# Kernel tuning notes

Hardware: AMD Instinct MI355X
Metric: run time of the kernel (lower is better)

Reference implementation:

```python
import jax, jax.numpy as jnp
import numpy as np

N = 50000          # nodes
E = 1_600_000      # edges (avg degree 32)
D = 128            # in_channels
H = 128            # hidden_channels
B = 4096           # batch_nodes
BETA = 0.5


def setup_inputs() -> dict:
    key = jax.random.key(0)
    ks = jax.random.split(key, 12)
    s = 1.0 / np.sqrt(D)
    inp = {
        "x": jax.random.normal(ks[0], (N, D), jnp.float32),
        "edge_index": jax.random.randint(ks[1], (2, E), 0, N, dtype=jnp.int64),
        "batch_nodes": jax.random.randint(ks[2], (B,), 0, N, dtype=jnp.int64),
        "labels": jax.random.randint(ks[3], (N,), 0, 2, dtype=jnp.int64),
        # GCNConv layer params (weight [in,out], bias [out])
        "W1": jax.random.uniform(ks[4], (D, H), jnp.float32, -s, s),
        "b1": jnp.zeros((H,), jnp.float32),
        "W2": jax.random.uniform(ks[5], (H, H), jnp.float32, -s, s),
        "b2": jnp.zeros((H,), jnp.float32),
        # Bilinear heads: weight [H,H] (out_features=1), scalar bias
        "W_ctx": jax.random.uniform(ks[6], (H, H), jnp.float32, -s, s),
        "b_ctx": jnp.zeros((), jnp.float32),
        "W_loc": jax.random.uniform(ks[7], (H, H), jnp.float32, -s, s),
        "b_loc": jnp.zeros((), jnp.float32),
    }
    return inp


def _gcn_conv(h, W, b, src, dst, n):
    """PyG GCNConv: linear transform, add self-loops, sym-normalized scatter-add."""
    h = h @ W  # [n, out]
    loop = jnp.arange(n, dtype=src.dtype)
    src_f = jnp.concatenate([src, loop])
    dst_f = jnp.concatenate([dst, loop])
    deg = jax.ops.segment_sum(jnp.ones_like(dst_f, dtype=h.dtype), dst_f, num_segments=n)
    dinv = jnp.where(deg > 0, jax.lax.rsqrt(deg), 0.0)
    norm = dinv[src_f] * dinv[dst_f]                      # [E+n]
    msg = h[src_f] * norm[:, None]                        # gather + scale
    out = jax.ops.segment_sum(msg, dst_f, num_segments=n)  # scatter-add
    return out + b


def _bce_logits(z, y):
    # mean(softplus(z) - z*y) == BCEWithLogits
    return jnp.mean(jax.nn.softplus(z) - z * y)


def reference(x, edge_index, batch_nodes, labels, W1, b1, W2, b2, W_ctx, b_ctx, W_loc, b_loc):
    src, dst = edge_index[0], edge_index[1]
    n = x.shape[0]
    layers = [(W1, b1), (W2, b2)]

    # eval mode: dropout is identity
    h = x
    for W, b in layers:
        h = jax.nn.relu(_gcn_conv(h, W, b, src, dst, n))

    gf = h[batch_nodes]                                   # [B, H]
    y = (labels[batch_nodes] == 1).astype(gf.dtype)       # [B]
    pos_cnt = jnp.sum(y)
    neg_cnt = y.shape[0] - pos_cnt
    pos_proto = (y[:, None] * gf).sum(0) / pos_cnt        # [H]

    # context bilinear head: z_i = gf_i^T W_ctx pos_proto + b (neg_sim is dead code in source)
    pos_sim = gf @ (W_ctx @ pos_proto) + b_ctx            # [B]
    ctx_loss = _bce_logits(pos_sim, y)

    # environment view: zero out batch nodes, re-run GCN stack (no dropout in source)
    masked_x = x.at[batch_nodes].set(0.0)
    env_h = masked_x
    for W, b in layers:
        env_h = jax.nn.relu(_gcn_conv(env_h, W, b, src, dst, n))
    env_f = env_h[batch_nodes]                            # [B, H]

    local_sim = jnp.einsum('nd,de,ne->n', env_f, W_loc, gf) + b_loc
    local_loss = _bce_logits(local_sim, 1.0 - y)

    total_loss = BETA * ctx_loss + (1.0 - BETA) * local_loss
    # source's guard: both classes present (true w.h.p. for random labels)
    total_loss = jnp.where((pos_cnt > 0) & (neg_cnt > 0), total_loss, 0.0)
    return gf, total_loss
```

## Files before the change

kernel.cpp:

```cpp
#include <hip/hip_runtime.h>
#include <math.h>

#define HID 128
#define CAP 12288
#define NBUCK_MAX 256
#define EPB 8192

typedef _Float16 h2v __attribute__((ext_vector_type(2)));
typedef _Float16 h8v __attribute__((ext_vector_type(8)));
typedef float f4v __attribute__((ext_vector_type(4)));

static inline int ceil_div(int a, int b) { return (a + b - 1) / b; }


__global__ __launch_bounds__(256) void k_setup(const float* __restrict__ W1, const float* __restrict__ W2,
                                               const float* __restrict__ Wl, _Float16* T1, _Float16* T2,
                                               _Float16* Tl, unsigned int* mask, int* bcur,
                                               float* part, float* pcnt_raw, float* lsums, int mw, int NB) {
    int b = blockIdx.x;
    int t = threadIdx.x;
    if (b < 192) {
        int which = b >> 6;
        int idx = (b & 63) * 256 + t;
        int k = idx >> 7, c = idx & 127;
        const float* S = (which == 0) ? W1 : ((which == 1) ? W2 : Wl);
        _Float16* D = (which == 0) ? T1 : ((which == 1) ? T2 : Tl);
        D[c * 128 + k] = (_Float16)S[idx];
    } else {
        int i = (b - 192) * 256 + t;
        if (i < mw) mask[i] = 0u;
        if (i < NB) bcur[i] = i * CAP;
        if (b == 192) {
            if (t < 128) part[t] = 0.f;
            else if (t == 128) pcnt_raw[0] = 0.f;
            else if (t < 131) lsums[t - 129] = 0.f;
        }
    }
}


__global__ __launch_bounds__(1024) void k_partA(const int* __restrict__ ei, int* __restrict__ bcur,
                                                unsigned int* __restrict__ ebuf,
                                                const int* __restrict__ batch, unsigned int* mask,
                                                int E, int B, int NB, int NBLKE) {
    if ((int)blockIdx.x >= NBLKE) {
        int i = ((int)blockIdx.x - NBLKE) * 1024 + threadIdx.x;
        if (i < B) { int nd = batch[i]; atomicOr(&mask[nd >> 5], 1u << (nd & 31)); }
        return;
    }
    __shared__ int lcnt[NBUCK_MAX];
    __shared__ int sc[NBUCK_MAX];
    __shared__ int lcur[NBUCK_MAX];
    __shared__ int gbase[NBUCK_MAX];
    __shared__ unsigned int se[EPB];
    int tid = threadIdx.x;
    if (tid < NBUCK_MAX) lcnt[tid] = 0;
    __syncthreads();
    int base = blockIdx.x * EPB;
    unsigned int pk[8];
    int bk[8];
#pragma unroll
    for (int j = 0; j < 8; ++j) {
        int e = base + tid + j * 1024;
        if (e < E) {
            int s = ei[e], d = ei[E + e];
            pk[j] = ((unsigned int)s << 8) | (unsigned int)(d & 255);
            bk[j] = d >> 8;
            atomicAdd(&lcnt[bk[j]], 1);
        } else bk[j] = -1;
    }
    __syncthreads();
    if (tid < NBUCK_MAX) sc[tid] = lcnt[tid];
    __syncthreads();
    for (int off = 1; off < NBUCK_MAX; off <<= 1) {
        int v = 0;
        if (tid < NBUCK_MAX && tid >= off) v = sc[tid - off];
        __syncthreads();
        if (tid < NBUCK_MAX) sc[tid] += v;
        __syncthreads();
    }
    if (tid < NBUCK_MAX) {
        int cc = lcnt[tid];
        int lo = sc[tid] - cc;
        lcur[tid] = lo;
        gbase[tid] = cc ? atomicAdd(&bcur[tid], cc) : 0;
    }
    __syncthreads();
#pragma unroll
    for (int j = 0; j < 8; ++j) {
        if (bk[j] >= 0) {
            int r = atomicAdd(&lcur[bk[j]], 1);
            se[r] = pk[j];
        }
    }
    __syncthreads();
    int wid = tid >> 6, lane = tid & 63;
    for (int b = wid; b < NB; b += 16) {
        int cc = lcnt[b];
        int lo = sc[b] - cc;
        int go = gbase[b];
        for (int i = lane; i < cc; i += 64) ebuf[go + i] = se[lo + i];
    }
}


__global__ __launch_bounds__(256) void k_csr(const unsigned int* __restrict__ ebuf, const int* __restrict__ bcur,
                                             const unsigned int* __restrict__ mask,
                                             float* __restrict__ sdinv, int* __restrict__ rs,
                                             int* __restrict__ degpk, unsigned int* __restrict__ csr, int N) {
    __shared__ unsigned int se[CAP];
    __shared__ int deg[256];
    __shared__ int fde[256];
    __shared__ int sc[256];
    __shared__ int cu[256];
    __shared__ int cf[256];
    int b = blockIdx.x, t = threadIdx.x;
    deg[t] = 0; fde[t] = 0;
    __syncthreads();
    int base = b * CAP;
    int ecnt = bcur[b] - base;
    for (int i = t; i < ecnt; i += 256) {
        unsigned int v = ebuf[base + i];
        int s = v >> 8;
        int fl = (mask[s >> 5] >> (s & 31)) & 1;
        se[i] = ((unsigned int)s << 9) | ((unsigned int)fl << 8) | (v & 255);
        atomicAdd(&deg[v & 255], 1);
        if (fl) atomicAdd(&fde[v & 255], 1);
    }
    __syncthreads();
    int dv = deg[t], fv = fde[t];
    int pv = (dv + 7) & ~7;
    sc[t] = pv;
    __syncthreads();
    for (int off = 1; off < 256; off <<= 1) {
        int v2 = (t >= off) ? sc[t - off] : 0;
        __syncthreads();
        sc[t] += v2;
        __syncthreads();
    }
    int r0 = base + sc[t] - pv;
    cu[t] = r0;
    cf[t] = r0 + (dv - fv);
    int node = b * 256 + t;
    if (node < N) {
        rs[node] = r0;
        degpk[node] = dv | (fv << 16);
        float di = rsqrtf((float)(dv + 1));
        if ((mask[node >> 5] >> (node & 31)) & 1) di = -di;
        sdinv[node] = di;
    }
    __syncthreads();
    for (int i = t; i < ecnt; i += 256) {
        unsigned int v = se[i];
        int d8 = v & 255;
        int p = ((v >> 8) & 1) ? atomicAdd(&cf[d8], 1) : atomicAdd(&cu[d8], 1);
        csr[p] = v >> 9;
    }
    if (node < N) {
        for (int j = dv; j < pv; ++j) csr[r0 + j] = (unsigned int)N;
    }
}


__global__ __launch_bounds__(256) void k_cast(const float* __restrict__ x, const float* __restrict__ sdinv,
                                              _Float16* __restrict__ xs, _Float16* __restrict__ H, int N) {
    int i = blockIdx.x * 256 + threadIdx.x;
    int nx = N * 16;
    if (i < nx) {
        int node = i >> 4;
        float da = fabsf(sdinv[node]);
        int o = i * 8;
        float4 a = *(const float4*)&x[o];
        float4 b = *(const float4*)&x[o + 4];
        h8v v;
        v[0] = (_Float16)(a.x * da); v[1] = (_Float16)(a.y * da);
        v[2] = (_Float16)(a.z * da); v[3] = (_Float16)(a.w * da);
        v[4] = (_Float16)(b.x * da); v[5] = (_Float16)(b.y * da);
        v[6] = (_Float16)(b.z * da); v[7] = (_Float16)(b.w * da);
        *(h8v*)&xs[o] = v;
    } else if (i < nx + 16) {
        *(h8v*)&xs[(size_t)i * 8] = (h8v){};
    } else if (i < nx + 16 + 32) {
        int j = i - (nx + 16);
        *(h8v*)&H[(size_t)2 * N * HID + j * 8] = (h8v){};
    }
}


__global__ __launch_bounds__(512) void k_layer1(const _Float16* __restrict__ xs, const int* __restrict__ rs,
                                                const int* __restrict__ degpk, const unsigned int* __restrict__ csr,
                                                const float* __restrict__ sdinv, const _Float16* __restrict__ W1T,
                                                const float* __restrict__ bias, _Float16* __restrict__ H, int N) {
    __shared__ __align__(16) _Float16 sWT[128 * 136];
    __shared__ __align__(16) _Float16 sAgg[64 * 136];
    __shared__ float sbias[128];
    __shared__ float sda[32];
    float* sC = (float*)sWT;

    int tid = threadIdx.x;
    int wave = tid >> 6, lane = tid & 63;
    int grp = lane >> 4, rl = lane & 15;

#pragma unroll
    for (int it = 0; it < 4; ++it) {
        int lin = (it * 512 + tid) * 8;
        int c = lin >> 7, k = lin & 127;
        *(h8v*)&sWT[c * 136 + k] = *(const h8v*)&W1T[lin];
    }
    if (tid < 128) sbias[tid] = bias[tid];
    if (tid < 32) {
        int nd = blockIdx.x * 32 + tid;
        sda[tid] = (nd < N) ? fabsf(sdinv[nd]) : 0.f;
    }

    int ch = rl * 8;
    int lg = wave * 4 + grp;
    int row = blockIdx.x * 32 + lg;
    bool ok = row < N;
    int p = 0, deg = 0, fd = 0;
    float sd = 0.f;
    h8v hs = {};
    if (ok) {
        p = rs[row];
        int dp = degpk[row];
        deg = dp & 0xffff; fd = dp >> 16;
        sd = sdinv[row];
        hs = *(const h8v*)&xs[(size_t)row * HID + ch];
    }
    int ud = deg - fd;
    int pd = (deg + 7) & ~7;
    int t1 = max(pd, __shfl_xor(pd, 16));
    int m  = max(t1, __shfl_xor(t1, 32));
    float U[8] = {}, F[8] = {};
    for (int i = 0; i < m; i += 16) {
        int id[16];
#pragma unroll
        for (int k = 0; k < 16; ++k) {
            int raw = (int)csr[p + i + k];
            id[k] = (i + k < pd) ? raw : N;
        }
        h8v h[16];
#pragma unroll
        for (int k = 0; k < 16; ++k) h[k] = *(const h8v*)&xs[(size_t)id[k] * HID + ch];
        h8v s0 = (h[0] + h[1]) + (h[2] + h[3]);
        h8v s1 = (h[4] + h[5]) + (h[6] + h[7]);
        h8v s2 = (h[8] + h[9]) + (h[10] + h[11]);
        h8v s3 = (h[12] + h[13]) + (h[14] + h[15]);
        h8v s  = (s0 + s1) + (s2 + s3);
#pragma unroll
        for (int j = 0; j < 8; ++j) U[j] += (float)s[j];
        if (i + 16 > ud) {
#pragma unroll
            for (int k = 0; k < 16; ++k) {
                if (i + k >= ud && i + k < deg) {
#pragma unroll
                    for (int j = 0; j < 8; ++j) F[j] += (float)h[k][j];
                }
            }
        }
    }
    {
        float da = fabsf(sd);
        float keep = (sd < 0.f) ? 0.f : 1.f;
        h8v lo = {}, hi = {};
        if (ok) {
#pragma unroll
            for (int j = 0; j < 8; ++j) {
                float f = (float)hs[j];
                lo[j] = (_Float16)(da * (U[j] + f));
                hi[j] = (_Float16)(da * (U[j] - F[j] + keep * f));
            }
        }
        *(h8v*)&sAgg[(2 * lg) * 136 + ch] = lo;
        *(h8v*)&sAgg[(2 * lg + 1) * 136 + ch] = hi;
    }
    __syncthreads();

    int g = lane >> 4;
    int rowtile = (wave & 3) * 16;
    int colbase = (wave >> 2) * 64;
    f4v acc[4];
#pragma unroll
    for (int cc = 0; cc < 4; ++cc) acc[cc] = (f4v){0.f, 0.f, 0.f, 0.f};
#pragma unroll
    for (int kb = 0; kb < 4; ++kb) {
        int k0 = kb * 32 + g * 8;
        h8v av = *(const h8v*)&sAgg[(rowtile + rl) * 136 + k0];
#pragma unroll
        for (int cc = 0; cc < 4; ++cc) {
            h8v bv = *(const h8v*)&sWT[(colbase + cc * 16 + rl) * 136 + k0];
            acc[cc] = __builtin_amdgcn_mfma_f32_16x16x32_f16(bv, av, acc[cc], 0, 0, 0);
        }
    }
    __syncthreads();

    int lrow = rowtile + rl;
    float dsc = sda[lrow >> 1];
#pragma unroll
    for (int cc = 0; cc < 4; ++cc) {
        f4v v = acc[cc];
        int col = colbase + cc * 16 + g * 4;
#pragma unroll
        for (int i2 = 0; i2 < 4; ++i2) v[i2] = fmaxf(v[i2] + sbias[col + i2], 0.f) * dsc;
        *(f4v*)&sC[lrow * 132 + col] = v;
    }
    __syncthreads();

    int sr = tid >> 3, ck = tid & 7;
    int gRow = blockIdx.x * 64 + sr;
    if (gRow < 2 * N) {
        const float* src = &sC[sr * 132 + ck * 16];
        h8v o0, o1;
#pragma unroll
        for (int j = 0; j < 8; ++j) { o0[j] = (_Float16)src[j]; o1[j] = (_Float16)src[8 + j]; }
        _Float16* dst = &H[(size_t)gRow * HID + ck * 16];
        *(h8v*)&dst[0] = o0;
        *(h8v*)&dst[8] = o1;
    }
}


__global__ __launch_bounds__(256) void k_layer2(const _Float16* __restrict__ H, const int* __restrict__ rs,
                                                const int* __restrict__ degpk, const unsigned int* __restrict__ csr,
                                                const float* __restrict__ sdinv, const int* __restrict__ batch,
                                                const int* __restrict__ labels,
                                                const _Float16* __restrict__ W2T, const float* __restrict__ bias,
                                                float* __restrict__ gf, _Float16* __restrict__ envh,
                                                float* __restrict__ yv, float* __restrict__ part,
                                                float* __restrict__ pcnt_raw, int B, int N) {
    __shared__ __align__(16) _Float16 sWT[128 * 136];
    __shared__ __align__(16) _Float16 sAgg[32 * 136];
    __shared__ float sbias[128];
    __shared__ float sy2[16];
    float* sC = (float*)sWT;

    int tid = threadIdx.x;
    int wave = tid >> 6, lane = tid & 63;
    int grp = lane >> 4, rl = lane & 15;

#pragma unroll
    for (int it = 0; it < 8; ++it) {
        int lin = (it * 256 + tid) * 8;
        int c = lin >> 7, k = lin & 127;
        *(h8v*)&sWT[c * 136 + k] = *(const h8v*)&W2T[lin];
    }
    if (tid < 128) sbias[tid] = bias[tid];

    int ch = rl * 8;
    int lg = wave * 4 + grp;
    int ri = blockIdx.x * 16 + lg;
    bool ok = ri < B;
    int p = 0, deg = 0, row = 0;
    float da = 0.f;
    h8v hn = {}, he = {};
    if (ok) {
        row = batch[ri];
        p = rs[row];
        deg = degpk[row] & 0xffff;
        da = fabsf(sdinv[row]);
        hn = *(const h8v*)&H[(size_t)row * 256 + ch];
        he = *(const h8v*)&H[(size_t)row * 256 + 128 + ch];
    }
    int pd = (deg + 7) & ~7;
    int t1 = max(pd, __shfl_xor(pd, 16));
    int m  = max(t1, __shfl_xor(t1, 32));
    float a[8] = {}, e[8] = {};
    for (int i = 0; i < m; i += 8) {
        int id[8];
#pragma unroll
        for (int k = 0; k < 8; ++k) {
            int raw = (int)csr[p + i + k];
            id[k] = (i + k < pd) ? raw : N;
        }
        h8v xn[8], xe[8];
#pragma unroll
        for (int k = 0; k < 8; ++k) {
            xn[k] = *(const h8v*)&H[(size_t)id[k] * 256 + ch];
            xe[k] = *(const h8v*)&H[(size_t)id[k] * 256 + 128 + ch];
        }
        h8v sn = ((xn[0] + xn[1]) + (xn[2] + xn[3])) + ((xn[4] + xn[5]) + (xn[6] + xn[7]));
        h8v sv = ((xe[0] + xe[1]) + (xe[2] + xe[3])) + ((xe[4] + xe[5]) + (xe[6] + xe[7]));
#pragma unroll
        for (int j = 0; j < 8; ++j) { a[j] += (float)sn[j]; e[j] += (float)sv[j]; }
    }
    {
        h8v lo = {}, hi = {};
        if (ok) {
#pragma unroll
            for (int j = 0; j < 8; ++j) {
                lo[j] = (_Float16)(da * (a[j] + (float)hn[j]));
                hi[j] = (_Float16)(da * (e[j] + (float)he[j]));
            }
        }
        *(h8v*)&sAgg[(2 * lg) * 136 + ch] = lo;
        *(h8v*)&sAgg[(2 * lg + 1) * 136 + ch] = hi;
    }
    __syncthreads();

    int g = lane >> 4;
    int rowtile = (wave & 1) * 16;
    int colbase = (wave >> 1) * 64;
    f4v acc[4];
#pragma unroll
    for (int cc = 0; cc < 4; ++cc) acc[cc] = (f4v){0.f, 0.f, 0.f, 0.f};
#pragma unroll
    for (int kb = 0; kb < 4; ++kb) {
        int k0 = kb * 32 + g * 8;
        h8v av = *(const h8v*)&sAgg[(rowtile + rl) * 136 + k0];
#pragma unroll
        for (int cc = 0; cc < 4; ++cc) {
            h8v bv = *(const h8v*)&sWT[(colbase + cc * 16 + rl) * 136 + k0];
            acc[cc] = __builtin_amdgcn_mfma_f32_16x16x32_f16(bv, av, acc[cc], 0, 0, 0);
        }
    }
    __syncthreads();

    int lrow = rowtile + rl;
#pragma unroll
    for (int cc = 0; cc < 4; ++cc) {
        f4v v = acc[cc];
        int col = colbase + cc * 16 + g * 4;
#pragma unroll
        for (int i2 = 0; i2 < 4; ++i2) v[i2] = fmaxf(v[i2] + sbias[col + i2], 0.f);
        *(f4v*)&sC[lrow * 132 + col] = v;
    }
    __syncthreads();

    int sr = tid >> 3, ck = tid & 7;
    int ri2 = blockIdx.x * 16 + (sr >> 1);
    if (ri2 < B) {
        const float* src = &sC[sr * 132 + ck * 16];
        if ((sr & 1) == 0) {
            float* dst = &gf[(size_t)ri2 * HID + ck * 16];
#pragma unroll
            for (int q = 0; q < 4; ++q) *(float4*)&dst[q * 4] = *(const float4*)&src[q * 4];
        } else {
            h8v o0, o1;
#pragma unroll
            for (int j = 0; j < 8; ++j) { o0[j] = (_Float16)src[j]; o1[j] = (_Float16)src[8 + j]; }
            _Float16* dst = &envh[(size_t)ri2 * HID + ck * 16];
            *(h8v*)&dst[0] = o0;
            *(h8v*)&dst[8] = o1;
        }
    }

    int rr = blockIdx.x * 16 + tid;
    if (tid < 16) {
        float y = 0.f;
        if (rr < B) {
            y = (labels[batch[rr]] == 1) ? 1.f : 0.f;
            yv[rr] = y;
        }
        sy2[tid] = y;
    }
    __syncthreads();
    if (tid < 128) {
        float acc2 = 0.f;
#pragma unroll
        for (int r2 = 0; r2 < 16; ++r2) acc2 += sy2[r2] * sC[(2 * r2) * 132 + tid];
        atomicAdd(&part[tid], acc2);
    } else if (tid == 128) {
        float ps = 0.f;
#pragma unroll
        for (int r2 = 0; r2 < 16; ++r2) ps += sy2[r2];
        atomicAdd(&pcnt_raw[0], ps);
    }
}


__global__ __launch_bounds__(128) void k_ctxvec(const float* __restrict__ Wctx, const float* __restrict__ part,
                                                const float* __restrict__ pcnt_raw, float* v) {
    __shared__ float sproto[128];
    int t = threadIdx.x;
    float pc = pcnt_raw[0];
    sproto[t] = part[t] / pc;
    __syncthreads();
    float acc = 0.f;
#pragma unroll 4
    for (int j = 0; j < 128; ++j) acc += Wctx[t * 128 + j] * sproto[j];
    v[t] = acc;
}


__global__ __launch_bounds__(256) void k_headsT(const _Float16* __restrict__ envh, const float* __restrict__ gf,
                                                const _Float16* __restrict__ WlT, const float* __restrict__ v,
                                                const float* __restrict__ yv, const float* __restrict__ bctx,
                                                const float* __restrict__ bloc, float* __restrict__ lsums, int B) {
    __shared__ __align__(16) _Float16 sWT[128 * 136];
    __shared__ float sv[128];
    int tid = threadIdx.x;
#pragma unroll
    for (int it = 0; it < 8; ++it) {
        int lin = (it * 256 + tid) * 8;
        int c = lin >> 7, k = lin & 127;
        *(h8v*)&sWT[c * 136 + k] = *(const h8v*)&WlT[lin];
    }
    if (tid < 128) sv[tid] = v[tid];
    __syncthreads();

    int wave = tid >> 6, lane = tid & 63;
    int rl = lane & 15, g = lane >> 4;
    int r = blockIdx.x * 64 + wave * 16 + rl;
    bool rok = r < B;
    f4v acc[8];
#pragma unroll
    for (int cf = 0; cf < 8; ++cf) acc[cf] = (f4v){0.f, 0.f, 0.f, 0.f};
#pragma unroll
    for (int kb = 0; kb < 4; ++kb) {
        int k0 = kb * 32 + g * 8;
        h8v av = {};
        if (rok) av = *(const h8v*)&envh[(size_t)r * HID + k0];
#pragma unroll
        for (int cf = 0; cf < 8; ++cf) {
            h8v bv = *(const h8v*)&sWT[(cf * 16 + rl) * 136 + k0];
            acc[cf] = __builtin_amdgcn_mfma_f32_16x16x32_f16(bv, av, acc[cf], 0, 0, 0);
        }
    }
    float s1 = 0.f, s2 = 0.f;
    if (rok) {
#pragma unroll
        for (int cf = 0; cf < 8; ++cf) {
            int col = cf * 16 + g * 4;
            float4 gv = *(const float4*)&gf[(size_t)r * HID + col];
            s2 += acc[cf][0] * gv.x + acc[cf][1] * gv.y + acc[cf][2] * gv.z + acc[cf][3] * gv.w;
            s1 += sv[col] * gv.x + sv[col + 1] * gv.y + sv[col + 2] * gv.z + sv[col + 3] * gv.w;
        }
    }
    s1 += __shfl_xor(s1, 16); s1 += __shfl_xor(s1, 32);
    s2 += __shfl_xor(s2, 16); s2 += __shfl_xor(s2, 32);
    float l1 = 0.f, l2 = 0.f;
    if (g == 0 && rok) {
        float y = yv[r];
        float z1 = s1 + bctx[0];
        float z2 = s2 + bloc[0];
        l1 = fmaxf(z1, 0.f) + log1pf(expf(-fabsf(z1))) - z1 * y;
        l2 = fmaxf(z2, 0.f) + log1pf(expf(-fabsf(z2))) - z2 * (1.f - y);
    }
#pragma unroll
    for (int o = 1; o < 64; o <<= 1) {
        l1 += __shfl_xor(l1, o);
        l2 += __shfl_xor(l2, o);
    }
    if (lane == 0) {
        atomicAdd(&lsums[0], l1);
        atomicAdd(&lsums[1], l2);
    }
}

__global__ void k_final(const float* __restrict__ lsums, const float* __restrict__ pcnt_raw,
                        float* out_loss, int B) {
    if (blockIdx.x == 0 && threadIdx.x == 0) {
        float pc = pcnt_raw[0];
        float nc = (float)B - pc;
        float total = 0.5f * (lsums[0] / (float)B) + 0.5f * (lsums[1] / (float)B);
        out_loss[0] = (pc > 0.f && nc > 0.f) ? total : 0.f;
    }
}


extern "C" void kernel_launch(void* const* d_in, const int* in_sizes, int n_in,
                              void* d_out, int out_size, void* d_ws, size_t ws_size,
                              hipStream_t stream) {
    const float* x      = (const float*)d_in[0];
    const int*   ei     = (const int*)d_in[1];
    const int*   batch  = (const int*)d_in[2];
    const int*   labels = (const int*)d_in[3];
    const float* W1     = (const float*)d_in[4];
    const float* b1     = (const float*)d_in[5];
    const float* W2     = (const float*)d_in[6];
    const float* b2     = (const float*)d_in[7];
    const float* Wctx   = (const float*)d_in[8];
    const float* bctx   = (const float*)d_in[9];
    const float* Wloc   = (const float*)d_in[10];
    const float* bloc   = (const float*)d_in[11];

    int N = in_sizes[0] / HID;
    int E = in_sizes[1] / 2;
    int B = in_sizes[2];
    float* out = (float*)d_out;

    char* wsb = (char*)d_ws;
    size_t off = 0;
    auto alloc = [&](size_t bytes) -> char* {
        char* p = wsb + off;
        off += (bytes + 255) & ~(size_t)255;
        return p;
    };
    int NB = ceil_div(N, 256);
    int mw = ceil_div(N, 32);

    _Float16* xs   = (_Float16*)alloc((size_t)(N + 1) * HID * 2);
    _Float16* H    = (_Float16*)alloc((size_t)(2 * N + 2) * HID * 2);
    unsigned int* ebuf = (unsigned int*)alloc((size_t)NB * CAP * 4);
    unsigned int* csr  = (unsigned int*)alloc((size_t)NB * CAP * 4);
    float* sdinv = (float*)alloc((size_t)N * 4);
    int*   rs    = (int*)alloc((size_t)N * 4);
    int*   degpk = (int*)alloc((size_t)N * 4);
    int*   bcur  = (int*)alloc((size_t)NB * 4);
    unsigned int* mask = (unsigned int*)alloc((size_t)mw * 4);
    _Float16* W1T = (_Float16*)alloc(128 * 128 * 2);
    _Float16* W2T = (_Float16*)alloc(128 * 128 * 2);
    _Float16* WlT = (_Float16*)alloc(128 * 128 * 2);
    _Float16* envh  = (_Float16*)alloc((size_t)B * HID * 2);
    float* yv    = (float*)alloc((size_t)B * 4);
    float* part  = (float*)alloc(128 * 4);
    float* pcnt_raw = (float*)alloc(256);
    float* lsums = (float*)alloc(256);
    float* vvec  = (float*)alloc(128 * 4);
    (void)ws_size; (void)n_in; (void)out_size;

    int NBLKE = ceil_div(E, EPB);
    int NBLKB = ceil_div(B, 1024);

    k_setup<<<192 + ceil_div(mw, 256), 256, 0, stream>>>(W1, W2, Wloc, W1T, W2T, WlT, mask, bcur,
                                                         part, pcnt_raw, lsums, mw, NB);
    k_partA<<<NBLKE + NBLKB, 1024, 0, stream>>>(ei, bcur, ebuf, batch, mask, E, B, NB, NBLKE);
    k_csr<<<NB, 256, 0, stream>>>(ebuf, bcur, mask, sdinv, rs, degpk, csr, N);
    k_cast<<<ceil_div(N * 16 + 48, 256), 256, 0, stream>>>(x, sdinv, xs, H, N);

    k_layer1<<<ceil_div(N, 32), 512, 0, stream>>>(xs, rs, degpk, csr, sdinv, W1T, b1, H, N);

    k_layer2<<<ceil_div(B, 16), 256, 0, stream>>>(H, rs, degpk, csr, sdinv, batch, labels, W2T, b2,
                                                  out, envh, yv, part, pcnt_raw, B, N);

    k_ctxvec<<<1, 128, 0, stream>>>(Wctx, part, pcnt_raw, vvec);
    k_headsT<<<ceil_div(B, 64), 256, 0, stream>>>(envh, out, WlT, vvec, yv, bctx, bloc, lsums, B);
    k_final<<<1, 1, 0, stream>>>(lsums, pcnt_raw, out + (size_t)B * HID, B);
}
```

Baseline: 146.4 us.

## Fold ctx-vector and final loss kernels into heads kernel; widen layer2 blocks

Removes the single-block k_ctxvec and k_final launches. Each k_headsT block now recomputes the Wctx·proto vector redundantly, and the last block to finish, found with an atomic counter, writes the final loss. Separately, k_layer2 moves to 512 threads so each 32-lane half-wave gathers one view (node or env) rather than both, which doubles gather parallelism per row and splits the MFMA work over 8 waves. This cuts two launch gaps and the serial tail latency, at the cost of redundant 128x128 matvecs per heads block and a threadfence/atomic epilogue.

```diff
diff --git a/kernel.cpp b/kernel.cpp
--- a/kernel.cpp
+++ b/kernel.cpp
@@ -16,7 +16,8 @@
 __global__ __launch_bounds__(256) void k_setup(const float* __restrict__ W1, const float* __restrict__ W2,
                                                const float* __restrict__ Wl, _Float16* T1, _Float16* T2,
                                                _Float16* Tl, unsigned int* mask, int* bcur,
-                                               float* part, float* pcnt_raw, float* lsums, int mw, int NB) {
+                                               float* part, float* pcnt_raw, float* lsums, int* donecnt,
+                                               int mw, int NB) {
     int b = blockIdx.x;
     int t = threadIdx.x;
     if (b < 192) {
@@ -34,6 +35,7 @@
             if (t < 128) part[t] = 0.f;
             else if (t == 128) pcnt_raw[0] = 0.f;
             else if (t < 131) lsums[t - 129] = 0.f;
+            else if (t == 131) donecnt[0] = 0;
         }
     }
 }
@@ -320,7 +322,7 @@
 }
 
 
-__global__ __launch_bounds__(256) void k_layer2(const _Float16* __restrict__ H, const int* __restrict__ rs,
+__global__ __launch_bounds__(512) void k_layer2(const _Float16* __restrict__ H, const int* __restrict__ rs,
                                                 const int* __restrict__ degpk, const unsigned int* __restrict__ csr,
                                                 const float* __restrict__ sdinv, const int* __restrict__ batch,
                                                 const int* __restrict__ labels,
@@ -336,35 +338,35 @@
 
     int tid = threadIdx.x;
     int wave = tid >> 6, lane = tid & 63;
-    int grp = lane >> 4, rl = lane & 15;
-
-#pragma unroll
-    for (int it = 0; it < 8; ++it) {
-        int lin = (it * 256 + tid) * 8;
+
+#pragma unroll
+    for (int it = 0; it < 4; ++it) {
+        int lin = (it * 512 + tid) * 8;
         int c = lin >> 7, k = lin & 127;
         *(h8v*)&sWT[c * 136 + k] = *(const h8v*)&W2T[lin];
     }
     if (tid < 128) sbias[tid] = bias[tid];
 
+    int rl32 = lane & 31;
+    int view = rl32 >> 4;
+    int rl = rl32 & 15;
     int ch = rl * 8;
-    int lg = wave * 4 + grp;
+    int lg = wave * 2 + (lane >> 5);
     int ri = blockIdx.x * 16 + lg;
     bool ok = ri < B;
     int p = 0, deg = 0, row = 0;
     float da = 0.f;
-    h8v hn = {}, he = {};
+    h8v hsv = {};
     if (ok) {
         row = batch[ri];
         p = rs[row];
         deg = degpk[row] & 0xffff;
         da = fabsf(sdinv[row]);
-        hn = *(const h8v*)&H[(size_t)row * 256 + ch];
-        he = *(const h8v*)&H[(size_t)row * 256 + 128 + ch];
+        hsv = *(const h8v*)&H[(size_t)row * 256 + view * 128 + ch];
     }
     int pd = (deg + 7) & ~7;
-    int t1 = max(pd, __shfl_xor(pd, 16));
-    int m  = max(t1, __shfl_xor(t1, 32));
-    float a[8] = {}, e[8] = {};
+    int m = max(pd, __shfl_xor(pd, 32));
+    float a[8] = {};
     for (int i = 0; i < m; i += 8) {
         int id[8];
 #pragma unroll
@@ -372,52 +374,45 @@
             int raw = (int)csr[p + i + k];
             id[k] = (i + k < pd) ? raw : N;
         }
-        h8v xn[8], xe[8];
-#pragma unroll
-        for (int k = 0; k < 8; ++k) {
-            xn[k] = *(const h8v*)&H[(size_t)id[k] * 256 + ch];
-            xe[k] = *(const h8v*)&H[(size_t)id[k] * 256 + 128 + ch];
-        }
-        h8v sn = ((xn[0] + xn[1]) + (xn[2] + xn[3])) + ((xn[4] + xn[5]) + (xn[6] + xn[7]));
-        h8v sv = ((xe[0] + xe[1]) + (xe[2] + xe[3])) + ((xe[4] + xe[5]) + (xe[6] + xe[7]));
-#pragma unroll
-        for (int j = 0; j < 8; ++j) { a[j] += (float)sn[j]; e[j] += (float)sv[j]; }
+        h8v x[8];
+#pragma unroll
+        for (int k = 0; k < 8; ++k) x[k] = *(const h8v*)&H[(size_t)id[k] * 256 + view * 128 + ch];
+        h8v s = ((x[0] + x[1]) + (x[2] + x[3])) + ((x[4] + x[5]) + (x[6] + x[7]));
+#pragma unroll
+        for (int j = 0; j < 8; ++j) a[j] += (float)s[j];
     }
     {
-        h8v lo = {}, hi = {};
+        h8v lo = {};
         if (ok) {
 #pragma unroll
-            for (int j = 0; j < 8; ++j) {
-                lo[j] = (_Float16)(da * (a[j] + (float)hn[j]));
-                hi[j] = (_Float16)(da * (e[j] + (float)he[j]));
-            }
-        }
-        *(h8v*)&sAgg[(2 * lg) * 136 + ch] = lo;
-        *(h8v*)&sAgg[(2 * lg + 1) * 136 + ch] = hi;
+            for (int j = 0; j < 8; ++j) lo[j] = (_Float16)(da * (a[j] + (float)hsv[j]));
+        }
+        *(h8v*)&sAgg[(2 * lg + view) * 136 + ch] = lo;
     }
     __syncthreads();
 
     int g = lane >> 4;
+    int rl2 = lane & 15;
     int rowtile = (wave & 1) * 16;
-    int colbase = (wave >> 1) * 64;
-    f4v acc[4];
-#pragma unroll
-    for (int cc = 0; cc < 4; ++cc) acc[cc] = (f4v){0.f, 0.f, 0.f, 0.f};
+    int colbase = (wave >> 1) * 32;
+    f4v acc[2];
+    acc[0] = (f4v){0.f, 0.f, 0.f, 0.f};
+    acc[1] = (f4v){0.f, 0.f, 0.f, 0.f};
 #pragma unroll
     for (int kb = 0; kb < 4; ++kb) {
         int k0 = kb * 32 + g * 8;
-        h8v av = *(const h8v*)&sAgg[(rowtile + rl) * 136 + k0];
-#pragma unroll
-        for (int cc = 0; cc < 4; ++cc) {
-            h8v bv = *(const h8v*)&sWT[(colbase + cc * 16 + rl) * 136 + k0];
+        h8v av = *(const h8v*)&sAgg[(rowtile + rl2) * 136 + k0];
+#pragma unroll
+        for (int cc = 0; cc < 2; ++cc) {
+            h8v bv = *(const h8v*)&sWT[(colbase + cc * 16 + rl2) * 136 + k0];
             acc[cc] = __builtin_amdgcn_mfma_f32_16x16x32_f16(bv, av, acc[cc], 0, 0, 0);
         }
     }
     __syncthreads();
 
-    int lrow = rowtile + rl;
-#pragma unroll
-    for (int cc = 0; cc < 4; ++cc) {
+    int lrow = rowtile + rl2;
+#pragma unroll
+    for (int cc = 0; cc < 2; ++cc) {
         f4v v = acc[cc];
         int col = colbase + cc * 16 + g * 4;
 #pragma unroll
@@ -426,21 +421,19 @@
     }
     __syncthreads();
 
-    int sr = tid >> 3, ck = tid & 7;
+    int sr = tid >> 4, ck = tid & 15;
     int ri2 = blockIdx.x * 16 + (sr >> 1);
     if (ri2 < B) {
-        const float* src = &sC[sr * 132 + ck * 16];
+        const float* src = &sC[sr * 132 + ck * 8];
         if ((sr & 1) == 0) {
-            float* dst = &gf[(size_t)ri2 * HID + ck * 16];
-#pragma unroll
-            for (int q = 0; q < 4; ++q) *(float4*)&dst[q * 4] = *(const float4*)&src[q * 4];
+            float* dst = &gf[(size_t)ri2 * HID + ck * 8];
+            *(float4*)&dst[0] = *(const float4*)&src[0];
+            *(float4*)&dst[4] = *(const float4*)&src[4];
         } else {
-            h8v o0, o1;
-#pragma unroll
-            for (int j = 0; j < 8; ++j) { o0[j] = (_Float16)src[j]; o1[j] = (_Float16)src[8 + j]; }
-            _Float16* dst = &envh[(size_t)ri2 * HID + ck * 16];
-            *(h8v*)&dst[0] = o0;
-            *(h8v*)&dst[8] = o1;
+            h8v o;
+#pragma unroll
+            for (int j = 0; j < 8; ++j) o[j] = (_Float16)src[j];
+            *(h8v*)&envh[(size_t)ri2 * HID + ck * 8] = o;
         }
     }
 
@@ -468,26 +461,16 @@
 }
 
 
-__global__ __launch_bounds__(128) void k_ctxvec(const float* __restrict__ Wctx, const float* __restrict__ part,
-                                                const float* __restrict__ pcnt_raw, float* v) {
-    __shared__ float sproto[128];
-    int t = threadIdx.x;
-    float pc = pcnt_raw[0];
-    sproto[t] = part[t] / pc;
-    __syncthreads();
-    float acc = 0.f;
-#pragma unroll 4
-    for (int j = 0; j < 128; ++j) acc += Wctx[t * 128 + j] * sproto[j];
-    v[t] = acc;
-}
-
-
 __global__ __launch_bounds__(256) void k_headsT(const _Float16* __restrict__ envh, const float* __restrict__ gf,
-                                                const _Float16* __restrict__ WlT, const float* __restrict__ v,
+                                                const _Float16* __restrict__ WlT, const float* __restrict__ Wctx,
+                                                const float* __restrict__ part, const float* __restrict__ pcnt_raw,
                                                 const float* __restrict__ yv, const float* __restrict__ bctx,
-                                                const float* __restrict__ bloc, float* __restrict__ lsums, int B) {
+                                                const float* __restrict__ bloc, float* __restrict__ lsums,
+                                                int* __restrict__ donecnt, float* __restrict__ out_loss,
+                                                int B, int nblk) {
     __shared__ __align__(16) _Float16 sWT[128 * 136];
     __shared__ float sv[128];
+    __shared__ float sproto[128];
     int tid = threadIdx.x;
 #pragma unroll
     for (int it = 0; it < 8; ++it) {
@@ -495,7 +478,14 @@
         int c = lin >> 7, k = lin & 127;
         *(h8v*)&sWT[c * 136 + k] = *(const h8v*)&WlT[lin];
     }
-    if (tid < 128) sv[tid] = v[tid];
+    if (tid < 128) sproto[tid] = part[tid] / pcnt_raw[0];
+    __syncthreads();
+    if (tid < 128) {
+        float acc = 0.f;
+#pragma unroll 4
+        for (int j = 0; j < 128; ++j) acc += Wctx[tid * 128 + j] * sproto[j];
+        sv[tid] = acc;
+    }
     __syncthreads();
 
     int wave = tid >> 6, lane = tid & 63;
@@ -545,15 +535,18 @@
         atomicAdd(&lsums[0], l1);
         atomicAdd(&lsums[1], l2);
     }
-}
-
-__global__ void k_final(const float* __restrict__ lsums, const float* __restrict__ pcnt_raw,
-                        float* out_loss, int B) {
-    if (blockIdx.x == 0 && threadIdx.x == 0) {
-        float pc = pcnt_raw[0];
-        float nc = (float)B - pc;
-        float total = 0.5f * (lsums[0] / (float)B) + 0.5f * (lsums[1] / (float)B);
-        out_loss[0] = (pc > 0.f && nc > 0.f) ? total : 0.f;
+    __syncthreads();
+    if (tid == 0) {
+        __threadfence();
+        int old = atomicAdd(donecnt, 1);
+        if (old == nblk - 1) {
+            float l1s = atomicAdd(&lsums[0], 0.f);
+            float l2s = atomicAdd(&lsums[1], 0.f);
+            float pc = pcnt_raw[0];
+            float nc = (float)B - pc;
+            float total = 0.5f * (l1s / (float)B) + 0.5f * (l2s / (float)B);
+            out_loss[0] = (pc > 0.f && nc > 0.f) ? total : 0.f;
+        }
     }
 }
 
@@ -606,24 +599,24 @@
     float* part  = (float*)alloc(128 * 4);
     float* pcnt_raw = (float*)alloc(256);
     float* lsums = (float*)alloc(256);
-    float* vvec  = (float*)alloc(128 * 4);
+    int*   donecnt = (int*)alloc(256);
     (void)ws_size; (void)n_in; (void)out_size;
 
     int NBLKE = ceil_div(E, EPB);
     int NBLKB = ceil_div(B, 1024);
+    int NHB = ceil_div(B, 64);
 
     k_setup<<<192 + ceil_div(mw, 256), 256, 0, stream>>>(W1, W2, Wloc, W1T, W2T, WlT, mask, bcur,
-                                                         part, pcnt_raw, lsums, mw, NB);
+                                                         part, pcnt_raw, lsums, donecnt, mw, NB);
     k_partA<<<NBLKE + NBLKB, 1024, 0, stream>>>(ei, bcur, ebuf, batch, mask, E, B, NB, NBLKE);
     k_csr<<<NB, 256, 0, stream>>>(ebuf, bcur, mask, sdinv, rs, degpk, csr, N);
     k_cast<<<ceil_div(N * 16 + 48, 256), 256, 0, stream>>>(x, sdinv, xs, H, N);
 
     k_layer1<<<ceil_div(N, 32), 512, 0, stream>>>(xs, rs, degpk, csr, sdinv, W1T, b1, H, N);
 
-    k_layer2<<<ceil_div(B, 16), 256, 0, stream>>>(H, rs, degpk, csr, sdinv, batch, labels, W2T, b2,
+    k_layer2<<<ceil_div(B, 16), 512, 0, stream>>>(H, rs, degpk, csr, sdinv, batch, labels, W2T, b2,
                                                   out, envh, yv, part, pcnt_raw, B, N);
 
-    k_ctxvec<<<1, 128, 0, stream>>>(Wctx, part, pcnt_raw, vvec);
-    k_headsT<<<ceil_div(B, 64), 256, 0, stream>>>(envh, out, WlT, vvec, yv, bctx, bloc, lsums, B);
-    k_final<<<1, 1, 0, stream>>>(lsums, pcnt_raw, out + (size_t)B * HID, B);
-}
+    k_headsT<<<NHB, 256, 0, stream>>>(envh, out, WlT, Wctx, part, pcnt_raw, yv, bctx, bloc,
+                                      lsums, donecnt, out + (size_t)B * HID, B, NHB);
+}
```

Result: no change. 144.2 us (-1.5%).
